# Kernel optimization log

Measured on AMD Instinct MI355X. Metric: run time of the kernel, lower is better.

Reference implementation:

```python
import jax, jax.numpy as jnp
import numpy as np

B = 4096      # batch
H = 512       # hidden_size
V = 512       # vocab_size
T = 31        # max_length + 1
D_IN = 14     # linear_in input features


def setup_inputs() -> dict:
    key = jax.random.key(0)
    ks = jax.random.split(key, 6)
    sc = 1.0 / np.sqrt(H).astype(np.float32)
    return {
        "inputs": jax.random.normal(ks[0], (B, D_IN), jnp.float32),
        "W_in": jax.random.normal(ks[1], (H, D_IN), jnp.float32) * (1.0 / np.sqrt(D_IN).astype(np.float32)),
        "b_in": jnp.zeros((H,), jnp.float32),
        "W_ih": jax.random.normal(ks[2], (3 * H, H), jnp.float32) * sc,
        "b_ih": jnp.zeros((3 * H,), jnp.float32),
        "W_hh": jax.random.normal(ks[3], (3 * H, H), jnp.float32) * sc,
        "b_hh": jnp.zeros((3 * H,), jnp.float32),
        "W_out": jax.random.normal(ks[4], (V, H), jnp.float32) * sc,
        "b_out": jnp.zeros((V,), jnp.float32),
    }


def reference(inputs, W_in, b_in, W_ih, b_ih, W_hh, b_hh, W_out, b_out):
    batch = inputs.shape[0]
    x = inputs @ W_in.T + b_in                     # [B,H]
    # Input projection is loop-invariant (same x fed every step in the original)
    gi = x @ W_ih.T + b_ih                         # [B,3H]
    gi_r, gi_z, gi_n = jnp.split(gi, 3, axis=1)

    def step(h, _):
        gh = h @ W_hh.T + b_hh                     # [B,3H]
        gh_r, gh_z, gh_n = jnp.split(gh, 3, axis=1)
        r = jax.nn.sigmoid(gi_r + gh_r)
        z = jax.nn.sigmoid(gi_z + gh_z)
        n = jnp.tanh(gi_n + r * gh_n)
        h_new = (1.0 - z) * n + z * h              # PyTorch GRUCell update
        return h_new, h_new

    h0 = jnp.zeros((batch, W_hh.shape[1]), x.dtype)
    _, hs = jax.lax.scan(step, h0, None, length=T)  # [T,B,H]
    hs = jnp.transpose(hs, (1, 0, 2))               # [B,T,H]
    logits = jnp.einsum('bth,vh->btv', hs, W_out) + b_out  # [B,T,V]
    outputs = jax.nn.softmax(logits, axis=2)
    hidden_flat = hs.reshape(batch, -1)             # [B,T*H]
    return outputs, hidden_flat
```

## Files before the change

### kernel.cpp

```cpp
#include <hip/hip_runtime.h>

#define NTH 15872

typedef __bf16 bf16x8 __attribute__((ext_vector_type(8)));
typedef float  f32x4  __attribute__((ext_vector_type(4)));

__device__ __forceinline__ unsigned short f2bf(float f) {
    unsigned u = __float_as_uint(f);
    u = u + 0x7fffu + ((u >> 16) & 1u);
    return (unsigned short)(u >> 16);
}
__device__ __forceinline__ float sigm(float x)  { return 1.f / (1.f + __expf(-x)); }
__device__ __forceinline__ float tanhf_(float x){ return 2.f / (1.f + __expf(-2.f * x)) - 1.f; }

__device__ __forceinline__ int lds_off(int r, int kb) {
    return r * 64 + ((kb ^ ((r >> 1) & 3)) << 4);
}
__device__ __forceinline__ int4 ldg16(const char* g0, int stride, int kbyte, int c) {
    int r = c >> 2, kb = c & 3;
    return *(const int4*)(g0 + (size_t)r * stride + kbyte + kb * 16);
}
__device__ __forceinline__ void sts16(char* lds, int c, int4 v) {
    int r = c >> 2, kb = c & 3;
    *(int4*)(lds + lds_off(r, kb)) = v;
}
__device__ __forceinline__ bf16x8 ldsfrag(const char* lds, int row, int hi) {
    return *(const bf16x8*)(lds + lds_off(row, hi));
}
__device__ __forceinline__ int4 ldg16_f32(const float* g0, int stride, int koff, int c) {
    int r = c >> 2, kb = c & 3;
    const float4* p = (const float4*)(g0 + (size_t)r * stride + koff + kb * 8);
    float4 a = p[0], b = p[1];
    union { unsigned short us[8]; int4 v; } u;
    u.us[0]=f2bf(a.x); u.us[1]=f2bf(a.y); u.us[2]=f2bf(a.z); u.us[3]=f2bf(a.w);
    u.us[4]=f2bf(b.x); u.us[5]=f2bf(b.y); u.us[6]=f2bf(b.z); u.us[7]=f2bf(b.w);
    return u.v;
}

__global__ void k_f32_to_bf16(const float* __restrict__ in,
                              unsigned short* __restrict__ out, int n4) {
    int i = blockIdx.x * 256 + threadIdx.x;
    if (i < n4) {
        float4 v = ((const float4*)in)[i];
        ushort4 o;
        o.x = f2bf(v.x); o.y = f2bf(v.y); o.z = f2bf(v.z); o.w = f2bf(v.w);
        ((ushort4*)out)[i] = o;
    }
}

__global__ void k_linear_in(const float* __restrict__ inp,
                            const float* __restrict__ W,
                            const float* __restrict__ bias,
                            unsigned short* __restrict__ xb)
{
    int idx = blockIdx.x * 256 + threadIdx.x;
    int b = idx >> 9, j = idx & 511;
    const float* ir = inp + (size_t)b * 14;
    const float* wr = W + (size_t)j * 14;
    float acc = bias[j];
#pragma unroll
    for (int k = 0; k < 14; ++k) acc += ir[k] * wr[k];
    xb[idx] = f2bf(acc);
}

__global__ __launch_bounds__(256) void k_gemm_gi(
    const unsigned short* __restrict__ A,
    const unsigned short* __restrict__ W,
    const float* __restrict__ bias,
    float* __restrict__ C)
{
    __shared__ __align__(16) char lA[128 * 64];
    __shared__ __align__(16) char lB[64 * 64];
    const int tid = threadIdx.x, lane = tid & 63, wid = tid >> 6;
    const int wm = wid >> 1, wn = wid & 1, hi = lane >> 4, c16 = lane & 15;
    const int m0 = blockIdx.x * 128, n0 = blockIdx.y * 64;
    const char* ga = (const char*)(A + (size_t)m0 * 512);
    const char* gb = (const char*)(W + (size_t)n0 * 512);
    f32x4 acc[4][2] = {};
    int4 ra0 = ldg16(ga, 1024, 0, tid);
    int4 ra1 = ldg16(ga, 1024, 0, tid + 256);
    int4 rb0 = ldg16(gb, 1024, 0, tid);
    for (int kt = 0; kt < 16; ++kt) {
        if (kt) __syncthreads();
        sts16(lA, tid, ra0); sts16(lA, tid + 256, ra1); sts16(lB, tid, rb0);
        __syncthreads();
        if (kt < 15) {
            int kb = (kt + 1) * 64;
            ra0 = ldg16(ga, 1024, kb, tid);
            ra1 = ldg16(ga, 1024, kb, tid + 256);
            rb0 = ldg16(gb, 1024, kb, tid);
        }
        bf16x8 af[4];
#pragma unroll
        for (int i = 0; i < 4; ++i) af[i] = ldsfrag(lA, wm * 64 + i * 16 + c16, hi);
#pragma unroll
        for (int j = 0; j < 2; ++j) {
            bf16x8 bfr = ldsfrag(lB, wn * 32 + j * 16 + c16, hi);
#pragma unroll
            for (int i = 0; i < 4; ++i)
                acc[i][j] = __builtin_amdgcn_mfma_f32_16x16x32_bf16(af[i], bfr, acc[i][j], 0, 0, 0);
        }
    }
#pragma unroll
    for (int i = 0; i < 4; ++i) {
        int m = m0 + wm * 64 + i * 16 + hi * 4;
#pragma unroll
        for (int j = 0; j < 2; ++j) {
            int n = n0 + wn * 32 + j * 16 + c16;
            float bj = bias[n];
#pragma unroll
            for (int q = 0; q < 4; ++q)
                C[(size_t)(m + q) * 1536 + n] = acc[i][j][q] + bj;
        }
    }
}

__device__ __forceinline__ int4 ldg16B3v(const char* gW, int n0, int kbyte, int c) {
    int r = c >> 2, kb = c & 3;
    int wrow = ((r >> 5) << 9) + n0 + (r & 31);
    return *(const int4*)(gW + (size_t)wrow * 1024 + kbyte + kb * 16);
}

__global__ __launch_bounds__(256) void k_step(
    const unsigned short* __restrict__ Hin, int hstride,
    const unsigned short* __restrict__ Whh,
    const float* __restrict__ gi,
    const float* __restrict__ bhh,
    float* __restrict__ hidden,
    unsigned short* __restrict__ Hout, int ostride,
    int t)
{
    __shared__ __align__(16) char lA[2][128 * 64];
    __shared__ __align__(16) char lB[2][96 * 64];
    const int tid = threadIdx.x, lane = tid & 63, wid = tid >> 6;
    const int wm = wid >> 1, wn = wid & 1, hi = lane >> 4, c16 = lane & 15;
    const int m0 = blockIdx.x * 128, n0 = blockIdx.y * 32;
    f32x4 acc[3][4] = {};
    if (t > 0) {
        const char* ga = (const char*)(Hin + (size_t)m0 * hstride);
        const int gas = hstride * 2;
        const char* gw = (const char*)Whh;
        int4 ra0 = ldg16(ga, gas, 0, tid);
        int4 ra1 = ldg16(ga, gas, 0, tid + 256);
        int4 rb0 = ldg16B3v(gw, n0, 0, tid);
        int4 rb1;
        if (tid < 128) rb1 = ldg16B3v(gw, n0, 0, tid + 256);
        sts16(lA[0], tid, ra0); sts16(lA[0], tid + 256, ra1);
        sts16(lB[0], tid, rb0);
        if (tid < 128) sts16(lB[0], tid + 256, rb1);
        for (int kt = 0; kt < 16; ++kt) {
            const int cur = kt & 1;
            if (kt < 15) {
                int kb = (kt + 1) * 64;
                ra0 = ldg16(ga, gas, kb, tid);
                ra1 = ldg16(ga, gas, kb, tid + 256);
                rb0 = ldg16B3v(gw, n0, kb, tid);
                if (tid < 128) rb1 = ldg16B3v(gw, n0, kb, tid + 256);
            }
            __syncthreads();
            bf16x8 af[4];
#pragma unroll
            for (int i = 0; i < 4; ++i) af[i] = ldsfrag(lA[cur], wm * 64 + i * 16 + c16, hi);
#pragma unroll
            for (int g = 0; g < 3; ++g) {
                bf16x8 bfr = ldsfrag(lB[cur], g * 32 + wn * 16 + c16, hi);
#pragma unroll
                for (int i = 0; i < 4; ++i)
                    acc[g][i] = __builtin_amdgcn_mfma_f32_16x16x32_bf16(af[i], bfr, acc[g][i], 0, 0, 0);
            }
            if (kt < 15) {
                sts16(lA[cur ^ 1], tid, ra0); sts16(lA[cur ^ 1], tid + 256, ra1);
                sts16(lB[cur ^ 1], tid, rb0);
                if (tid < 128) sts16(lB[cur ^ 1], tid + 256, rb1);
            }
        }
    }
    const int n = n0 + wn * 16 + c16;
    const float br = bhh[n], bz = bhh[512 + n], bn_ = bhh[1024 + n];
#pragma unroll
    for (int i = 0; i < 4; ++i) {
        int mB = m0 + wm * 64 + i * 16 + hi * 4;
#pragma unroll
        for (int q = 0; q < 4; ++q) {
            int m = mB + q;
            size_t gb0 = (size_t)m * 1536 + n;
            float pr = gi[gb0]        + acc[0][i][q] + br;
            float pz = gi[gb0 + 512]  + acc[1][i][q] + bz;
            float r  = sigm(pr);
            float z  = sigm(pz);
            float nn = tanhf_(gi[gb0 + 1024] + r * (acc[2][i][q] + bn_));
            float hold = (t > 0) ? hidden[(size_t)m * NTH + (size_t)(t - 1) * 512 + n] : 0.f;
            float hn = (1.f - z) * nn + z * hold;
            hidden[(size_t)m * NTH + (size_t)t * 512 + n] = hn;
            Hout[(size_t)m * ostride + n] = f2bf(hn);
        }
    }
}

template<bool BF16A>
__global__ __launch_bounds__(256) void k_proj(
    const void* __restrict__ Aptr,
    int astr,
    const unsigned short* __restrict__ Wo,
    const float* __restrict__ bo,
    float* __restrict__ out)
{
    __shared__ __align__(16) char lA[64 * 64];
    __shared__ __align__(16) char lB[512 * 64];
    __shared__ float red[2][2][32];
    const int tid = threadIdx.x, lane = tid & 63, wid = tid >> 6;
    const int wm = wid >> 1, wn = wid & 1, hi = lane >> 4, c16 = lane & 15;
    const int m0 = blockIdx.x * 64;
    const char*  gab = (const char*)Aptr  + (size_t)m0 * astr * 2;
    const float* gaf = (const float*)Aptr + (size_t)m0 * astr;
    const char*  gb  = (const char*)Wo;
    f32x4 acc[2][16] = {};
    int4 ra = BF16A ? ldg16(gab, astr * 2, 0, tid) : ldg16_f32(gaf, astr, 0, tid);
    int4 rb[8];
#pragma unroll
    for (int s = 0; s < 8; ++s) rb[s] = ldg16(gb, 1024, 0, tid + 256 * s);
    for (int kt = 0; kt < 16; ++kt) {
        if (kt) __syncthreads();
        sts16(lA, tid, ra);
#pragma unroll
        for (int s = 0; s < 8; ++s) sts16(lB, tid + 256 * s, rb[s]);
        __syncthreads();
        if (kt < 15) {
            ra = BF16A ? ldg16(gab, astr * 2, (kt + 1) * 64, tid)
                       : ldg16_f32(gaf, astr, (kt + 1) * 32, tid);
#pragma unroll
            for (int s = 0; s < 8; ++s) rb[s] = ldg16(gb, 1024, (kt + 1) * 64, tid + 256 * s);
        }
        bf16x8 af[2];
#pragma unroll
        for (int mf = 0; mf < 2; ++mf)
            af[mf] = ldsfrag(lA, wm * 32 + mf * 16 + c16, hi);
#pragma unroll
        for (int nf = 0; nf < 16; ++nf) {
            bf16x8 bfr = ldsfrag(lB, wn * 256 + nf * 16 + c16, hi);
#pragma unroll
            for (int mf = 0; mf < 2; ++mf)
                acc[mf][nf] = __builtin_amdgcn_mfma_f32_16x16x32_bf16(af[mf], bfr, acc[mf][nf], 0, 0, 0);
        }
    }
#pragma unroll
    for (int nf = 0; nf < 16; ++nf) {
        float bj = bo[wn * 256 + nf * 16 + c16];
#pragma unroll
        for (int mf = 0; mf < 2; ++mf)
#pragma unroll
            for (int q = 0; q < 4; ++q)
                acc[mf][nf][q] = __expf(acc[mf][nf][q] + bj);
    }
#pragma unroll
    for (int mf = 0; mf < 2; ++mf)
#pragma unroll
        for (int q = 0; q < 4; ++q) {
            float s = 0.f;
#pragma unroll
            for (int nf = 0; nf < 16; ++nf) s += acc[mf][nf][q];
            s += __shfl_xor(s, 1); s += __shfl_xor(s, 2);
            s += __shfl_xor(s, 4); s += __shfl_xor(s, 8);
            if (c16 == 0) red[wm][wn][mf * 16 + hi * 4 + q] = s;
        }
    __syncthreads();
#pragma unroll
    for (int mf = 0; mf < 2; ++mf)
#pragma unroll
        for (int q = 0; q < 4; ++q) {
            int rl = mf * 16 + hi * 4 + q;
            float inv = 1.f / (red[wm][0][rl] + red[wm][1][rl]);
            int m = m0 + wm * 32 + rl;
            float* orow = out + (size_t)m * 512 + wn * 256 + c16;
#pragma unroll
            for (int nf = 0; nf < 16; ++nf) orow[nf * 16] = acc[mf][nf][q] * inv;
        }
}

extern "C" void kernel_launch(void* const* d_in, const int* in_sizes, int n_in,
                              void* d_out, int out_size, void* d_ws, size_t ws_size,
                              hipStream_t stream) {
    const float* inputs = (const float*)d_in[0];
    const float* W_in   = (const float*)d_in[1];
    const float* b_in   = (const float*)d_in[2];
    const float* W_ih   = (const float*)d_in[3];
    const float* b_ih   = (const float*)d_in[4];
    const float* W_hh   = (const float*)d_in[5];
    const float* b_hh   = (const float*)d_in[6];
    const float* W_out  = (const float*)d_in[7];
    const float* b_out  = (const float*)d_in[8];

    float* out    = (float*)d_out;
    float* hidden = out + (size_t)126976 * 512;

    char* ws = (char*)d_ws;
    unsigned short* wih_b  = (unsigned short*)(ws);
    unsigned short* whh_b  = (unsigned short*)(ws + 1572864);
    unsigned short* wout_b = (unsigned short*)(ws + 3145728);
    unsigned short* x_b    = (unsigned short*)(ws + 3670016);
    float*          gi     = (float*)(ws + 7864320);
    const bool big = ws_size >= 163053568ULL;
    unsigned short* hbf2   = (unsigned short*)(ws + 33030144);
    unsigned short* hb0    = (unsigned short*)(ws + 33030144);
    unsigned short* hb1    = (unsigned short*)(ws + 37224448);

    k_f32_to_bf16<<<768, 256, 0, stream>>>(W_ih, wih_b, 196608);
    k_f32_to_bf16<<<768, 256, 0, stream>>>(W_hh, whh_b, 196608);
    k_f32_to_bf16<<<256, 256, 0, stream>>>(W_out, wout_b, 65536);
    k_linear_in<<<8192, 256, 0, stream>>>(inputs, W_in, b_in, x_b);
    k_gemm_gi<<<dim3(32, 24), 256, 0, stream>>>(x_b, wih_b, b_ih, gi);

    for (int t = 0; t < 31; ++t) {
        const unsigned short* Hin;
        unsigned short* Hout;
        int hs, os;
        if (big) {
            Hin  = hbf2 + (size_t)(t > 0 ? t - 1 : 0) * 512;  hs = NTH;
            Hout = hbf2 + (size_t)t * 512;                     os = NTH;
        } else {
            Hin  = (t & 1) ? hb0 : hb1;  hs = 512;
            Hout = (t & 1) ? hb1 : hb0;  os = 512;
        }
        k_step<<<dim3(32, 16), 256, 0, stream>>>(Hin, hs, whh_b, gi, b_hh,
                                                 hidden, Hout, os, t);
    }
    if (big) k_proj<true><<<1984, 256, 0, stream>>>(hbf2, 512, wout_b, b_out, out);
    else     k_proj<false><<<1984, 256, 0, stream>>>(hidden, 512, wout_b, b_out, out);
}
```

Measured before the change: 782.6 us.

## Prepack W_hh into MFMA fragment order and load B fragments directly to registers

A new pre-pass converts W_hh to bf16 and stores it in the exact per-lane MFMA B-fragment order. The recurrent step kernel then loads its B operands with coalesced 16-byte global loads straight into registers, double-buffered across k-tiles. This removes the shared-memory staging of W_hh, its stores and reads. The cost is more registers per thread and some redundant global/L2 traffic, since each of the two wm waves loads the same fragments.

Measured after the change: 778.1 us. Within noise of the previous version (-0.6%).

```diff
diff --git a/kernel.cpp b/kernel.cpp
--- a/kernel.cpp
+++ b/kernel.cpp
@@ -27,14 +27,16 @@
 __device__ __forceinline__ bf16x8 ldsfrag(const char* lds, int row, int hi) {
     return *(const bf16x8*)(lds + lds_off(row, hi));
 }
-__device__ __forceinline__ int4 ldg16_f32(const float* g0, int stride, int koff, int c) {
-    int r = c >> 2, kb = c & 3;
-    const float4* p = (const float4*)(g0 + (size_t)r * stride + koff + kb * 8);
-    float4 a = p[0], b = p[1];
+__device__ __forceinline__ int4 pack8(const float* p) {
+    float4 a = ((const float4*)p)[0], b = ((const float4*)p)[1];
     union { unsigned short us[8]; int4 v; } u;
     u.us[0]=f2bf(a.x); u.us[1]=f2bf(a.y); u.us[2]=f2bf(a.z); u.us[3]=f2bf(a.w);
     u.us[4]=f2bf(b.x); u.us[5]=f2bf(b.y); u.us[6]=f2bf(b.z); u.us[7]=f2bf(b.w);
     return u.v;
+}
+__device__ __forceinline__ int4 ldg16_f32(const float* g0, int stride, int koff, int c) {
+    int r = c >> 2, kb = c & 3;
+    return pack8(g0 + (size_t)r * stride + koff + kb * 8);
 }
 
 __global__ void k_f32_to_bf16(const float* __restrict__ in,
@@ -46,6 +48,16 @@
         o.x = f2bf(v.x); o.y = f2bf(v.y); o.z = f2bf(v.z); o.w = f2bf(v.w);
         ((ushort4*)out)[i] = o;
     }
+}
+
+__global__ void k_wpack(const float* __restrict__ Whh, unsigned short* __restrict__ Wp) {
+    int cid = blockIdx.x * 256 + threadIdx.x;
+    int lane = cid & 63, c16 = lane & 15, hi = lane >> 4;
+    int wn = (cid >> 6) & 1, nb = (cid >> 7) & 15;
+    int v = cid >> 11;
+    int kt = v / 3, g = v - kt * 3;
+    int row = g * 512 + nb * 32 + wn * 16 + c16;
+    ((int4*)Wp)[cid] = pack8(Whh + (size_t)row * 512 + kt * 32 + hi * 8);
 }
 
 __global__ void k_linear_in(const float* __restrict__ inp,
@@ -115,15 +127,9 @@
     }
 }
 
-__device__ __forceinline__ int4 ldg16B3v(const char* gW, int n0, int kbyte, int c) {
-    int r = c >> 2, kb = c & 3;
-    int wrow = ((r >> 5) << 9) + n0 + (r & 31);
-    return *(const int4*)(gW + (size_t)wrow * 1024 + kbyte + kb * 16);
-}
-
 __global__ __launch_bounds__(256) void k_step(
     const unsigned short* __restrict__ Hin, int hstride,
-    const unsigned short* __restrict__ Whh,
+    const unsigned short* __restrict__ Wp,
     const float* __restrict__ gi,
     const float* __restrict__ bhh,
     float* __restrict__ hidden,
@@ -131,7 +137,6 @@
     int t)
 {
     __shared__ __align__(16) char lA[2][128 * 64];
-    __shared__ __align__(16) char lB[2][96 * 64];
     const int tid = threadIdx.x, lane = tid & 63, wid = tid >> 6;
     const int wm = wid >> 1, wn = wid & 1, hi = lane >> 4, c16 = lane & 15;
     const int m0 = blockIdx.x * 128, n0 = blockIdx.y * 32;
@@ -139,23 +144,24 @@
     if (t > 0) {
         const char* ga = (const char*)(Hin + (size_t)m0 * hstride);
         const int gas = hstride * 2;
-        const char* gw = (const char*)Whh;
+        const char* wp = (const char*)Wp + (size_t)(blockIdx.y * 2 + wn) * 1024 + lane * 16;
         int4 ra0 = ldg16(ga, gas, 0, tid);
         int4 ra1 = ldg16(ga, gas, 0, tid + 256);
-        int4 rb0 = ldg16B3v(gw, n0, 0, tid);
-        int4 rb1;
-        if (tid < 128) rb1 = ldg16B3v(gw, n0, 0, tid + 256);
+        bf16x8 Bf[2][3];
+#pragma unroll
+        for (int g = 0; g < 3; ++g)
+            Bf[0][g] = *(const bf16x8*)(wp + (size_t)g * 32768);
         sts16(lA[0], tid, ra0); sts16(lA[0], tid + 256, ra1);
-        sts16(lB[0], tid, rb0);
-        if (tid < 128) sts16(lB[0], tid + 256, rb1);
         for (int kt = 0; kt < 16; ++kt) {
             const int cur = kt & 1;
             if (kt < 15) {
                 int kb = (kt + 1) * 64;
                 ra0 = ldg16(ga, gas, kb, tid);
                 ra1 = ldg16(ga, gas, kb, tid + 256);
-                rb0 = ldg16B3v(gw, n0, kb, tid);
-                if (tid < 128) rb1 = ldg16B3v(gw, n0, kb, tid + 256);
+#pragma unroll
+                for (int g = 0; g < 3; ++g)
+                    Bf[(kt + 1) & 1][g] =
+                        *(const bf16x8*)(wp + (size_t)((kt + 1) * 3 + g) * 32768);
             }
             __syncthreads();
             bf16x8 af[4];
@@ -163,15 +169,12 @@
             for (int i = 0; i < 4; ++i) af[i] = ldsfrag(lA[cur], wm * 64 + i * 16 + c16, hi);
 #pragma unroll
             for (int g = 0; g < 3; ++g) {
-                bf16x8 bfr = ldsfrag(lB[cur], g * 32 + wn * 16 + c16, hi);
 #pragma unroll
                 for (int i = 0; i < 4; ++i)
-                    acc[g][i] = __builtin_amdgcn_mfma_f32_16x16x32_bf16(af[i], bfr, acc[g][i], 0, 0, 0);
+                    acc[g][i] = __builtin_amdgcn_mfma_f32_16x16x32_bf16(af[i], Bf[cur][g], acc[g][i], 0, 0, 0);
             }
             if (kt < 15) {
                 sts16(lA[cur ^ 1], tid, ra0); sts16(lA[cur ^ 1], tid + 256, ra1);
-                sts16(lB[cur ^ 1], tid, rb0);
-                if (tid < 128) sts16(lB[cur ^ 1], tid + 256, rb1);
             }
         }
     }
@@ -295,7 +298,7 @@
 
     char* ws = (char*)d_ws;
     unsigned short* wih_b  = (unsigned short*)(ws);
-    unsigned short* whh_b  = (unsigned short*)(ws + 1572864);
+    unsigned short* Wp     = (unsigned short*)(ws + 1572864);
     unsigned short* wout_b = (unsigned short*)(ws + 3145728);
     unsigned short* x_b    = (unsigned short*)(ws + 3670016);
     float*          gi     = (float*)(ws + 7864320);
@@ -305,7 +308,7 @@
     unsigned short* hb1    = (unsigned short*)(ws + 37224448);
 
     k_f32_to_bf16<<<768, 256, 0, stream>>>(W_ih, wih_b, 196608);
-    k_f32_to_bf16<<<768, 256, 0, stream>>>(W_hh, whh_b, 196608);
+    k_wpack<<<384, 256, 0, stream>>>(W_hh, Wp);
     k_f32_to_bf16<<<256, 256, 0, stream>>>(W_out, wout_b, 65536);
     k_linear_in<<<8192, 256, 0, stream>>>(inputs, W_in, b_in, x_b);
     k_gemm_gi<<<dim3(32, 24), 256, 0, stream>>>(x_b, wih_b, b_ih, gi);
@@ -321,7 +324,7 @@
             Hin  = (t & 1) ? hb0 : hb1;  hs = 512;
             Hout = (t & 1) ? hb1 : hb0;  os = 512;
         }
-        k_step<<<dim3(32, 16), 256, 0, stream>>>(Hin, hs, whh_b, gi, b_hh,
+        k_step<<<dim3(32, 16), 256, 0, stream>>>(Hin, hs, Wp, gi, b_hh,
                                                  hidden, Hout, os, t);
     }
     if (big) k_proj<true><<<1984, 256, 0, stream>>>(hbf2, 512, wout_b, b_out, out);
```
